# Optimization experiments

Measured on AMD Instinct MI355X. Metric: run time of the kernel, lower is better.

Reference implementation:

```python
import jax, jax.numpy as jnp
from jax import lax
import numpy as np

NSTEP, NGRID, MU = 365, 4000, 8
STAIND = NSTEP - 1          # time index providing static parameters
TDLST = [1, 2, 3, 4, 5]     # 1-based indices of dynamic parameters
HBV_LO = jnp.array([0.0, 1.0, 0.005, 0.005, 0.0, 0.0, 0.005, 0.005, 0.0, 0.0, 0.0], jnp.float32)
HBV_HI = jnp.array([1.0, 2000.0, 0.995, 0.995, 1.0, 7.0, 0.995, 0.995, 1.0, 1.0, 1.0], jnp.float32)
SMIN = 1e-4                 # clamp floor for states
CAPMIN = 0.005 / 4          # floor for derived capacities

# ---- MARRMoT-style flux helpers (all elementwise) ----

def split_1(p1, In):
    return p1 * In

def soilmoisture_1(S1, S1max, S2, S2max):
    mask = (S1 / S1max < S2 / S2max).astype(S1.dtype)
    return (S2 * S1max - S1 * S2max) / (S1max + S2max) * mask

def soilmoisture_2(S1, S1max, S2, S2max, S3, S3max):
    # water rebalance to equal relative storage (3 stores); flux drawn from S2
    mask = (S1 / S1max < (S2 + S3) / (S2max + S3max)).astype(S1.dtype)
    return (S2 * S1max - S1 * S2max) / (S1max + S2max + S3max) * mask

def evap_7(S, Smax, Ep, dt):
    return jnp.minimum(S / Smax * Ep, S / dt)

def evap_1(S, Ep, dt):
    return jnp.minimum(Ep, S / dt)

def saturation_1(In, S, Smax):
    return In * (S >= Smax).astype(In.dtype)

def interflow_5(p1, S):
    return p1 * S

def baseflow_1(p1, S):
    return p1 * S

def percolation_4(pbase, zperc, rexp, deficit, defmax, S, Smax, dt):
    pc = pbase * (1.0 + zperc * (deficit / defmax) ** (1.0 + rexp)) * S / Smax
    return jnp.maximum(0.0, jnp.minimum(pc, S / dt))

def deficit_dist(S1, S1max, S2, S2max):
    d1 = jnp.maximum(0.0, 1.0 - S1 / S1max)
    d2 = jnp.maximum(0.0, 1.0 - S2 / S2max)
    tot = d1 + d2
    return jnp.where(tot > 0, d1 / jnp.where(tot > 0, tot, 1.0), S1max / (S1max + S2max))


def _forward(x, parameters):
    Nstep, Ngrid = x.shape[0], x.shape[1]
    mu = parameters.shape[3]
    P_ = x[:, :, 0]   # [Nstep, Ngrid]
    Ep_ = x[:, :, 2]  # [Nstep, Ngrid]

    # scale raw [0,1] params to physical ranges
    parT = HBV_LO[None, None, :, None] + parameters * (HBV_HI - HBV_LO)[None, None, :, None]
    parsta = parT[STAIND]  # [Ngrid, 11, mu] static params
    dyn = np.zeros(11, dtype=bool)
    for ix in TDLST:
        dyn[ix - 1] = True
    dyn = jnp.asarray(dyn)
    # dydrop=0 -> dynamic params always used on tdlst slots, static elsewhere
    parhbv = jnp.where(dyn[None, None, :, None], parT, parsta[None])  # [Nstep,Ngrid,11,mu]

    S0 = jnp.full((Ngrid, mu), 0.001, x.dtype)

    def step(carry, inp):
        S1, S2, S3, S4, S5 = carry
        Pt, Ept, par = inp            # par: [Ngrid, 11, mu]
        P = Pt[:, None]               # [Ngrid, 1] broadcasts against [Ngrid, mu]
        Ep = Ept[:, None]
        pctim, smax, f1, f2, kuz, rexp, f3, f4, pfree, klzp, klzs = [par[:, i, :] for i in range(11)]

        uztwm = f1 * smax
        uzfwm = jnp.maximum(CAPMIN, f2 * (smax - uztwm))
        lztwm = jnp.maximum(CAPMIN, f3 * (smax - uztwm - uzfwm))
        lzfwpm = jnp.maximum(CAPMIN, f4 * (smax - uztwm - uzfwm - lztwm))
        lzfwsm = jnp.maximum(CAPMIN, (1.0 - f4) * (smax - uztwm - uzfwm - lztwm))
        pbase = lzfwpm * klzp + lzfwsm * klzs
        denom = lzfwsm * klzs + lzfwpm * klzp
        zperc = jnp.minimum(1e5, (lztwm + lzfwsm * (1.0 - klzs)) / denom + lzfwpm * (1.0 - klzp) / denom)
        dt = 1.0

        flux_qdir = split_1(pctim, P)
        flux_peff = split_1(1.0 - pctim, P)
        flux_ru = soilmoisture_1(S1, uztwm, S2, uzfwm)
        flux_euztw = evap_7(S1, uztwm, Ep, dt)
        flux_twexu = saturation_1(flux_peff, S1, uztwm)
        flux_qsur = saturation_1(flux_twexu, S2, uzfwm)
        flux_qint = interflow_5(kuz, S2)
        flux_euzfw = evap_1(S2, jnp.maximum(0.0, Ep - flux_euztw), dt)
        deficit = (jnp.maximum(1e-8, lztwm - S3) + jnp.maximum(1e-8, lzfwpm - S4)
                   + jnp.maximum(1e-8, lzfwsm - S5))
        defmax = jnp.maximum(1e-8, lztwm + lzfwpm + lzfwsm)
        flux_pc = percolation_4(pbase, zperc, rexp, deficit, defmax, S2, uzfwm, dt)
        flux_pctw = split_1(1.0 - pfree, flux_pc)
        flux_elztw = evap_7(S3, lztwm, jnp.maximum(0.0, Ep - flux_euztw - flux_euzfw), dt)
        flux_twexl = saturation_1(flux_pctw, S3, lztwm)
        fp = deficit_dist(S4, lzfwpm, S5, lzfwsm)
        fs = deficit_dist(S5, lzfwsm, S4, lzfwpm)
        flux_twexlp = split_1(fp, flux_twexl)
        flux_twexls = split_1(fs, flux_twexl)
        flux_pcfwp = split_1(pfree * fp, flux_pc)
        flux_pcfws = split_1(pfree * fs, flux_pc)
        flux_rlp = soilmoisture_2(S3, lztwm, S4, lzfwpm, S5, lzfwsm)
        flux_rls = soilmoisture_2(S3, lztwm, S5, lzfwsm, S4, lzfwpm)
        flux_qbfp = baseflow_1(klzp, S4)
        flux_qbfs = baseflow_1(klzs, S5)

        nS1 = jnp.maximum(S1 + flux_peff + flux_ru - flux_euztw - flux_twexu, SMIN)
        nS2 = jnp.maximum(S2 + flux_twexu - flux_euzfw - flux_qsur - flux_qint - flux_ru - flux_pc, SMIN)
        nS3 = jnp.maximum(S3 + flux_pctw + flux_rlp + flux_rls - flux_elztw - flux_twexl, SMIN)
        nS4 = jnp.maximum(S4 + flux_twexlp + flux_pcfwp - flux_rlp - flux_qbfp, SMIN)
        nS5 = jnp.maximum(S5 + flux_twexls + flux_pcfws - flux_rls - flux_qbfs, SMIN)

        qsim = flux_qdir + flux_qsur + flux_qint + flux_qbfp + flux_qbfs
        et = flux_euztw + flux_euzfw + flux_elztw
        return (nS1, nS2, nS3, nS4, nS5), (qsim, et)

    _, (Qsimmu, ETmu) = lax.scan(step, (S0, S0, S0, S0, S0), (P_, Ep_, parhbv))
    Qs = Qsimmu.mean(-1, keepdims=True)      # muwts=None -> mean over components
    ETave = ETmu.mean(-1, keepdims=True)
    return jnp.concatenate([Qs, ETave], axis=-1)  # [Nstep, Ngrid, 2]


def setup_inputs() -> dict:
    key = jax.random.key(0)
    k1, k2 = jax.random.split(key)
    x = jax.random.uniform(k1, (NSTEP, NGRID, 3), dtype=jnp.float32)
    parameters = jax.random.uniform(k2, (NSTEP, NGRID, 11, MU), dtype=jnp.float32)
    return {"x": x, "parameters": parameters}


def reference(x, parameters):
    return _forward(x, parameters)
```

## Files before the change

### kernel.cpp

```cpp
#include <hip/hip_runtime.h>
#include <stdint.h>

#define NSTEP 365
#define NGRID 4000
#define CAPMIN 0.00125f
#define SMINV 0.0001f
#define PSTR_DW (NGRID * 88)
#define XSTR_DW (NGRID * 3)

#define RAW_SLOT 384
#define RAW_REG  (5 * RAW_SLOT)
#define DER_BASE 7680
#define DER_SLOT 768
#define DER_REG  (5 * DER_SLOT)
#define SMQ_BASE 15360
#define SME_BASE 15680

typedef __attribute__((address_space(3))) uint32_t lds_u32_t;
typedef __attribute__((address_space(1))) uint32_t glb_u32_t;

__device__ __forceinline__ void dma4(const float* g, float* l) {
    __builtin_amdgcn_global_load_lds((const glb_u32_t*)(const void*)g,
                                     (lds_u32_t*)(void*)l, 4, 0, 0);
}

__device__ __forceinline__ float frcp(float x) { return __builtin_amdgcn_rcpf(x); }
__device__ __forceinline__ float fexp2(float x) { return __builtin_amdgcn_exp2f(x); }
__device__ __forceinline__ float flog2(float x) { return __builtin_amdgcn_logf(x); }

__device__ __forceinline__ void issue_slot(const float* pp, const float* px,
                                           int t, float* dst) {
    const float* pj = pp + (size_t)t * PSTR_DW;
    dma4(pj,      dst);
    dma4(pj + 8,  dst + 64);
    dma4(pj + 16, dst + 128);
    dma4(pj + 24, dst + 192);
    dma4(pj + 32, dst + 256);
    dma4(px + (size_t)t * XSTR_DW, dst + 320);
}

#define RDS(j)                                                               \
    const float  c0_##j = rreg[(j) * RAW_SLOT + lane];                       \
    const float  kz_##j = rreg[(j) * RAW_SLOT + 256 + lane];                 \
    const float  Pp_##j = rreg[(j) * RAW_SLOT + 320 + gl3];                  \
    const float  Ee_##j = rreg[(j) * RAW_SLOT + 322 + gl3];                  \
    const float2 dA_##j = dreg[(j) * 384 + lane];                            \
    const float2 dB_##j = dreg[(j) * 384 + 64 + lane];                       \
    const float2 dC_##j = dreg[(j) * 384 + 128 + lane];                      \
    const float2 dD_##j = dreg[(j) * 384 + 192 + lane];                      \
    const float2 dE_##j = dreg[(j) * 384 + 256 + lane];                      \
    const float2 dF_##j = dreg[(j) * 384 + 320 + lane];

#define STEP(j) do {                                                         \
    const float uztwm = dA_##j.x, uzfwm = dA_##j.y;                          \
    const float inv_uztwm = dB_##j.x, inv_uzfwm = dB_##j.y;                  \
    const float inv_uzsum = dC_##j.x, lztwm = dC_##j.y;                      \
    const float inv_lztwm = dD_##j.x, pbase = dD_##j.y;                      \
    const float lzfwpm = dE_##j.x, lzfwsm = dE_##j.y;                        \
    const float pz = dF_##j.x, inv_defmax = dF_##j.y;                        \
    const float Ep = Ee_##j, kuz = kz_##j;                                   \
    const float qdir = c0_##j * Pp_##j;                                      \
    const float peff = Pp_##j - qdir;                                        \
    const float rud  = S2 * uztwm - S1 * uzfwm;                              \
    const float ru   = (rud > 0.0f) ? rud * inv_uzsum : 0.0f;                \
    const float euztw = fminf(S1 * inv_uztwm * Ep, S1);                      \
    const float twexu = (S1 >= uztwm) ? peff : 0.0f;                         \
    const float qsur  = (S2 >= uzfwm) ? twexu : 0.0f;                        \
    const float qint  = kuz * S2;                                            \
    const float euzfw = fminf(fmaxf(0.0f, Ep - euztw), S2);                  \
    const float deficit = fmaxf(1e-8f, lztwm - S3)                           \
                        + fmaxf(1e-8f, lzfwpm - S4)                          \
                        + fmaxf(1e-8f, lzfwsm - S5);                         \
    const float powterm = fexp2(e1 * flog2(deficit * inv_defmax));           \
    float pc = (pbase + pz * powterm) * (S2 * inv_uzfwm);                    \
    pc = fmaxf(0.0f, fminf(pc, S2));                                         \
    const float pctw  = (1.0f - pfree) * pc;                                 \
    const float elztw = fminf(S3 * inv_lztwm                                 \
                              * fmaxf(0.0f, Ep - euztw - euzfw), S3);        \
    const float twexl = (S3 >= lztwm) ? pctw : 0.0f;                         \
    const float aa  = fmaxf(0.0f, lzfwpm - S4) * lzfwsm;                     \
    const float bb  = fmaxf(0.0f, lzfwsm - S5) * lzfwpm;                     \
    const float den = aa + bb;                                               \
    const float pm  = lzfwpm + lzfwsm;                                       \
    const float fp  = ((den > 0.0f) ? aa : lzfwpm)                           \
                    * frcp((den > 0.0f) ? den : pm);                         \
    const float fs  = 1.0f - fp;                                             \
    const float twexlp = fp * twexl;                                         \
    const float twexls = fs * twexl;                                         \
    const float pcfwp  = pfree * fp * pc;                                    \
    const float pcfws  = pfree * fs * pc;                                    \
    const bool rlm = S3 * pm < (S4 + S5) * lztwm;                            \
    const float rlp = rlm ? (S4 * lztwm - S3 * lzfwpm) * inv_defmax : 0.0f;  \
    const float rls = rlm ? (S5 * lztwm - S3 * lzfwsm) * inv_defmax : 0.0f;  \
    const float qbfp = klzp * S4;                                            \
    const float qbfs = klzs * S5;                                            \
    S1 = fmaxf(S1 + peff + ru - euztw - twexu, SMINV);                       \
    S2 = fmaxf(S2 + twexu - euzfw - qsur - qint - ru - pc, SMINV);           \
    S3 = fmaxf(S3 + pctw + rlp + rls - elztw - twexl, SMINV);                \
    S4 = fmaxf(S4 + twexlp + pcfwp - rlp - qbfp, SMINV);                     \
    S5 = fmaxf(S5 + twexls + pcfws - rls - qbfs, SMINV);                     \
    smq[(j) * 64 + lane] = qdir + qsur + qint + qbfp + qbfs;                 \
    sme[(j) * 64 + lane] = euztw + euzfw + elztw;                            \
} while (0)

__global__ __launch_bounds__(192, 1) void sacsma_kernel(
    const float* __restrict__ x,
    const float* __restrict__ par,
    float* __restrict__ out)
{
    __shared__ __align__(16) float lds[16000];

    const int wave = threadIdx.x >> 6;
    const int lane = threadIdx.x & 63;
    const int g0   = blockIdx.x * 8;
    const int gl   = lane >> 3;
    const int mu   = lane & 7;
    const int g    = g0 + gl;

    if (wave == 0) {
        const float* pp = par + (size_t)g * 88 + mu;
        int xl = lane; if (xl >= 24) xl -= 24; if (xl >= 24) xl -= 24;
        const int xq = xl / 3;
        const float* px = x + (g0 + xq) * 3 + (xl - xq * 3);

        #pragma unroll
        for (int j = 0; j < 5; ++j)
            issue_slot(pp, px, j, lds + j * RAW_SLOT);

        for (int i = 0; i < 75; ++i) {
            if (i <= 71) {
                const int b = i + 1;
                float* dst = lds + (b & 3) * RAW_REG;
                const int tb = 5 * b;
                #pragma unroll
                for (int j = 0; j < 5; ++j)
                    issue_slot(pp, px, tb + j, dst + j * RAW_SLOT);
                asm volatile("s_waitcnt vmcnt(30)" ::: "memory");
            } else {
                asm volatile("s_waitcnt vmcnt(0)" ::: "memory");
            }
            asm volatile("s_barrier" ::: "memory");
        }
    } else if (wave == 1) {
        const float* ps = par + ((size_t)(NSTEP - 1) * NGRID + g) * 88 + mu;
        const float f3   = 0.005f + ps[6 * 8] * 0.99f;
        const float f4   = 0.005f + ps[7 * 8] * 0.99f;
        const float klzp = ps[9 * 8];
        const float klzs = ps[10 * 8];

        for (int i = 0; i < 75; ++i) {
            if (i >= 1 && i <= 73) {
                const int b = i - 1;
                const float* rreg = lds + (b & 3) * RAW_REG;
                float* dregf = lds + DER_BASE + (b & 1) * DER_REG;
                #pragma unroll
                for (int j = 0; j < 5; ++j) {
                    const float* rb = rreg + j * RAW_SLOT;
                    float2* db = reinterpret_cast<float2*>(dregf + j * DER_SLOT);

                    const float c1 = rb[64 + lane];
                    const float c2 = rb[128 + lane];
                    const float c3 = rb[192 + lane];

                    const float smaxv = 1.0f + c1 * 1999.0f;
                    const float f1 = 0.005f + c2 * 0.99f;
                    const float f2 = 0.005f + c3 * 0.99f;
                    const float uztwm = f1 * smaxv;
                    float rem = smaxv - uztwm;
                    const float uzfwm = fmaxf(CAPMIN, f2 * rem);
                    rem -= uzfwm;
                    const float lztwm = fmaxf(CAPMIN, f3 * rem);
                    rem -= lztwm;
                    const float lzfwpm = fmaxf(CAPMIN, f4 * rem);
                    const float lzfwsm = fmaxf(CAPMIN, (1.0f - f4) * rem);
                    const float pbase = lzfwpm * klzp + lzfwsm * klzs;
                    const float pz = fminf(lztwm + lzfwsm * (1.0f - klzs)
                                           + lzfwpm * (1.0f - klzp),
                                           100000.0f * pbase);
                    const float inv_uztwm = frcp(uztwm);
                    const float inv_uzfwm = frcp(uzfwm);
                    const float inv_lztwm = frcp(lztwm);
                    const float inv_uzsum = frcp(uztwm + uzfwm);
                    const float inv_defmax = frcp(lztwm + lzfwpm + lzfwsm);

                    db[0 * 64 + lane] = make_float2(uztwm, uzfwm);
                    db[1 * 64 + lane] = make_float2(inv_uztwm, inv_uzfwm);
                    db[2 * 64 + lane] = make_float2(inv_uzsum, lztwm);
                    db[3 * 64 + lane] = make_float2(inv_lztwm, pbase);
                    db[4 * 64 + lane] = make_float2(lzfwpm, lzfwsm);
                    db[5 * 64 + lane] = make_float2(pz, inv_defmax);
                }
                asm volatile("s_waitcnt lgkmcnt(0)" ::: "memory");
            }
            asm volatile("s_barrier" ::: "memory");
        }
    } else {
        const float* ps = par + ((size_t)(NSTEP - 1) * NGRID + g) * 88 + mu;
        const float e1    = 1.0f + ps[5 * 8] * 7.0f;
        const float pfree = ps[8 * 8];
        const float klzp  = ps[9 * 8];
        const float klzs  = ps[10 * 8];

        float S1 = 0.001f, S2 = 0.001f, S3 = 0.001f, S4 = 0.001f, S5 = 0.001f;
        float* smq = lds + SMQ_BASE;
        float* sme = lds + SME_BASE;
        const int gl3 = gl * 3;

        for (int i = 0; i < 75; ++i) {
            if (i >= 2) {
                const int b = i - 2;
                const float* rreg = lds + (b & 3) * RAW_REG;
                const float2* dreg = reinterpret_cast<const float2*>(
                    lds + DER_BASE + (b & 1) * DER_REG);

                RDS(0) RDS(1) RDS(2) RDS(3) RDS(4)
                STEP(0); STEP(1); STEP(2); STEP(3); STEP(4);

                if (lane < 40) {
                    const int s  = lane >> 3;
                    const int gg = lane & 7;
                    const float4* q4 = reinterpret_cast<const float4*>(&smq[s * 64 + gg * 8]);
                    const float4* e4 = reinterpret_cast<const float4*>(&sme[s * 64 + gg * 8]);
                    const float4 qa = q4[0], qb = q4[1];
                    const float4 ea = e4[0], eb = e4[1];
                    const float qsum = ((qa.x + qa.y) + (qa.z + qa.w))
                                     + ((qb.x + qb.y) + (qb.z + qb.w));
                    const float esum = ((ea.x + ea.y) + (ea.z + ea.w))
                                     + ((eb.x + eb.y) + (eb.z + eb.w));
                    float2 o = make_float2(qsum * 0.125f, esum * 0.125f);
                    *reinterpret_cast<float2*>(
                        out + ((size_t)(5 * b + s) * NGRID + g0 + gg) * 2) = o;
                }
            }
            asm volatile("s_barrier" ::: "memory");
        }
    }
}

extern "C" void kernel_launch(void* const* d_in, const int* in_sizes, int n_in,
                              void* d_out, int out_size, void* d_ws, size_t ws_size,
                              hipStream_t stream) {
    const float* x   = (const float*)d_in[0];
    const float* par = (const float*)d_in[1];
    float* out = (float*)d_out;

    sacsma_kernel<<<NGRID / 8, 192, 0, stream>>>(x, par, out);
}
```

Baseline: 106.5 us.

## Move output reduction to loader wave, compact x DMA, set wave priorities

The per-batch mean-over-mu reduction and global store move from the serial compute wave to the loader wave. They read a double-buffered LDS staging area three iterations later. The x forcing loads are packed into two DMA instructions per batch instead of five, with a tighter LDS layout, and wave priorities are set so the compute wave gets issue preference. A redundant fmax(0) clamp on percolation is dropped. This shortens the critical recurrence path, at the cost of more complex LDS buffer lifetimes and a final drain store.

New measurement: 128.2 us (median of 2 runs). 20.4% more time.

```diff
diff --git a/kernel.cpp b/kernel.cpp
--- a/kernel.cpp
+++ b/kernel.cpp
@@ -8,13 +8,13 @@
 #define PSTR_DW (NGRID * 88)
 #define XSTR_DW (NGRID * 3)
 
-#define RAW_SLOT 384
-#define RAW_REG  (5 * RAW_SLOT)
-#define DER_BASE 7680
+#define RAW_REG  1728
+#define X_OFF    1600
+#define DER_BASE 6912
 #define DER_SLOT 768
-#define DER_REG  (5 * DER_SLOT)
-#define SMQ_BASE 15360
-#define SME_BASE 15680
+#define DER_REG  3840
+#define STG_BASE 14592
+#define STG_REG  640
 
 typedef __attribute__((address_space(3))) uint32_t lds_u32_t;
 typedef __attribute__((address_space(1))) uint32_t glb_u32_t;
@@ -28,22 +28,11 @@
 __device__ __forceinline__ float fexp2(float x) { return __builtin_amdgcn_exp2f(x); }
 __device__ __forceinline__ float flog2(float x) { return __builtin_amdgcn_logf(x); }
 
-__device__ __forceinline__ void issue_slot(const float* pp, const float* px,
-                                           int t, float* dst) {
-    const float* pj = pp + (size_t)t * PSTR_DW;
-    dma4(pj,      dst);
-    dma4(pj + 8,  dst + 64);
-    dma4(pj + 16, dst + 128);
-    dma4(pj + 24, dst + 192);
-    dma4(pj + 32, dst + 256);
-    dma4(px + (size_t)t * XSTR_DW, dst + 320);
-}
-
 #define RDS(j)                                                               \
-    const float  c0_##j = rreg[(j) * RAW_SLOT + lane];                       \
-    const float  kz_##j = rreg[(j) * RAW_SLOT + 256 + lane];                 \
-    const float  Pp_##j = rreg[(j) * RAW_SLOT + 320 + gl3];                  \
-    const float  Ee_##j = rreg[(j) * RAW_SLOT + 322 + gl3];                  \
+    const float  c0_##j = rreg[(j) * 320 + lane];                            \
+    const float  kz_##j = rreg[(j) * 320 + 256 + lane];                      \
+    const float  Pp_##j = xreg[(j) * 24 + gl3];                              \
+    const float  Ee_##j = xreg[(j) * 24 + gl3 + 2];                          \
     const float2 dA_##j = dreg[(j) * 384 + lane];                            \
     const float2 dB_##j = dreg[(j) * 384 + 64 + lane];                       \
     const float2 dC_##j = dreg[(j) * 384 + 128 + lane];                      \
@@ -72,8 +61,7 @@
                         + fmaxf(1e-8f, lzfwpm - S4)                          \
                         + fmaxf(1e-8f, lzfwsm - S5);                         \
     const float powterm = fexp2(e1 * flog2(deficit * inv_defmax));           \
-    float pc = (pbase + pz * powterm) * (S2 * inv_uzfwm);                    \
-    pc = fmaxf(0.0f, fminf(pc, S2));                                         \
+    const float pc = fminf((pbase + pz * powterm) * (S2 * inv_uzfwm), S2);   \
     const float pctw  = (1.0f - pfree) * pc;                                 \
     const float elztw = fminf(S3 * inv_lztwm                                 \
                               * fmaxf(0.0f, Ep - euztw - euzfw), S3);        \
@@ -99,8 +87,8 @@
     S3 = fmaxf(S3 + pctw + rlp + rls - elztw - twexl, SMINV);                \
     S4 = fmaxf(S4 + twexlp + pcfwp - rlp - qbfp, SMINV);                     \
     S5 = fmaxf(S5 + twexls + pcfws - rls - qbfs, SMINV);                     \
-    smq[(j) * 64 + lane] = qdir + qsur + qint + qbfp + qbfs;                 \
-    sme[(j) * 64 + lane] = euztw + euzfw + elztw;                            \
+    stq[(j) * 64 + lane] = qdir + qsur + qint + qbfp + qbfs;                 \
+    stq[320 + (j) * 64 + lane] = euztw + euzfw + elztw;                      \
 } while (0)
 
 __global__ __launch_bounds__(192, 1) void sacsma_kernel(
@@ -108,7 +96,7 @@
     const float* __restrict__ par,
     float* __restrict__ out)
 {
-    __shared__ __align__(16) float lds[16000];
+    __shared__ __align__(16) float lds[15872];
 
     const int wave = threadIdx.x >> 6;
     const int lane = threadIdx.x & 63;
@@ -118,30 +106,69 @@
     const int g    = g0 + gl;
 
     if (wave == 0) {
+        __builtin_amdgcn_s_setprio(0);
         const float* pp = par + (size_t)g * 88 + mu;
-        int xl = lane; if (xl >= 24) xl -= 24; if (xl >= 24) xl -= 24;
-        const int xq = xl / 3;
-        const float* px = x + (g0 + xq) * 3 + (xl - xq * 3);
-
-        #pragma unroll
-        for (int j = 0; j < 5; ++j)
-            issue_slot(pp, px, j, lds + j * RAW_SLOT);
-
-        for (int i = 0; i < 75; ++i) {
-            if (i <= 71) {
-                const int b = i + 1;
-                float* dst = lds + (b & 3) * RAW_REG;
-                const int tb = 5 * b;
-                #pragma unroll
-                for (int j = 0; j < 5; ++j)
-                    issue_slot(pp, px, tb + j, dst + j * RAW_SLOT);
-                asm volatile("s_waitcnt vmcnt(30)" ::: "memory");
+        const int tA = lane / 24;
+        const int rA = lane - 24 * tA;
+        int idxB = lane + 64;
+        int tB = idxB / 24;
+        int rB = idxB - 24 * tB;
+        if (tB > 4) { tB = 4; rB = idxB - 120; }
+        const float* pxA = x + (size_t)tA * XSTR_DW + g0 * 3 + rA;
+        const float* pxB = x + (size_t)tB * XSTR_DW + g0 * 3 + rB;
+
+        #define ISSUE_BATCH(b) do {                                          \
+            float* reg_ = lds + ((b) & 3) * RAW_REG;                         \
+            const int tb_ = 5 * (b);                                         \
+            _Pragma("unroll")                                                \
+            for (int j = 0; j < 5; ++j) {                                    \
+                const float* pj_ = pp + (size_t)(tb_ + j) * PSTR_DW;         \
+                float* dst_ = reg_ + j * 320;                                \
+                dma4(pj_,      dst_);                                        \
+                dma4(pj_ + 8,  dst_ + 64);                                   \
+                dma4(pj_ + 16, dst_ + 128);                                  \
+                dma4(pj_ + 24, dst_ + 192);                                  \
+                dma4(pj_ + 32, dst_ + 256);                                  \
+            }                                                                \
+            dma4(pxA + (size_t)tb_ * XSTR_DW, reg_ + X_OFF);                 \
+            dma4(pxB + (size_t)tb_ * XSTR_DW, reg_ + X_OFF + 64);            \
+        } while (0)
+
+        #define REDUCE_STORE(b) do {                                         \
+            if (lane < 40) {                                                 \
+                const float* stg_ = lds + STG_BASE + ((b) & 1) * STG_REG;    \
+                const int s_  = lane >> 3;                                   \
+                const int gg_ = lane & 7;                                    \
+                const float4 qa = *(const float4*)&stg_[s_ * 64 + gg_ * 8];  \
+                const float4 qb = *(const float4*)&stg_[s_ * 64 + gg_ * 8 + 4];\
+                const float4 ea = *(const float4*)&stg_[320 + s_ * 64 + gg_ * 8];\
+                const float4 eb = *(const float4*)&stg_[320 + s_ * 64 + gg_ * 8 + 4];\
+                const float qsum = ((qa.x + qa.y) + (qa.z + qa.w))           \
+                                 + ((qb.x + qb.y) + (qb.z + qb.w));          \
+                const float esum = ((ea.x + ea.y) + (ea.z + ea.w))           \
+                                 + ((eb.x + eb.y) + (eb.z + eb.w));          \
+                float2 o = make_float2(qsum * 0.125f, esum * 0.125f);        \
+                *reinterpret_cast<float2*>(                                   \
+                    out + ((size_t)(5 * (b) + s_) * NGRID + g0 + gg_) * 2) = o;\
+            }                                                                \
+        } while (0)
+
+        ISSUE_BATCH(0);
+
+        for (int ip = 0; ip < 75; ++ip) {
+            if (ip >= 3)
+                REDUCE_STORE(ip - 3);
+            if (ip <= 71) {
+                ISSUE_BATCH(ip + 1);
+                asm volatile("s_waitcnt vmcnt(27)" ::: "memory");
             } else {
                 asm volatile("s_waitcnt vmcnt(0)" ::: "memory");
             }
             asm volatile("s_barrier" ::: "memory");
         }
+        REDUCE_STORE(72);
     } else if (wave == 1) {
+        __builtin_amdgcn_s_setprio(1);
         const float* ps = par + ((size_t)(NSTEP - 1) * NGRID + g) * 88 + mu;
         const float f3   = 0.005f + ps[6 * 8] * 0.99f;
         const float f4   = 0.005f + ps[7 * 8] * 0.99f;
@@ -155,7 +182,7 @@
                 float* dregf = lds + DER_BASE + (b & 1) * DER_REG;
                 #pragma unroll
                 for (int j = 0; j < 5; ++j) {
-                    const float* rb = rreg + j * RAW_SLOT;
+                    const float* rb = rreg + j * 320;
                     float2* db = reinterpret_cast<float2*>(dregf + j * DER_SLOT);
 
                     const float c1 = rb[64 + lane];
@@ -195,6 +222,7 @@
             asm volatile("s_barrier" ::: "memory");
         }
     } else {
+        __builtin_amdgcn_s_setprio(2);
         const float* ps = par + ((size_t)(NSTEP - 1) * NGRID + g) * 88 + mu;
         const float e1    = 1.0f + ps[5 * 8] * 7.0f;
         const float pfree = ps[8 * 8];
@@ -202,35 +230,21 @@
         const float klzs  = ps[10 * 8];
 
         float S1 = 0.001f, S2 = 0.001f, S3 = 0.001f, S4 = 0.001f, S5 = 0.001f;
-        float* smq = lds + SMQ_BASE;
-        float* sme = lds + SME_BASE;
         const int gl3 = gl * 3;
 
         for (int i = 0; i < 75; ++i) {
             if (i >= 2) {
                 const int b = i - 2;
                 const float* rreg = lds + (b & 3) * RAW_REG;
+                const float* xreg = rreg + X_OFF;
                 const float2* dreg = reinterpret_cast<const float2*>(
                     lds + DER_BASE + (b & 1) * DER_REG);
+                float* stq = lds + STG_BASE + (b & 1) * STG_REG;
 
                 RDS(0) RDS(1) RDS(2) RDS(3) RDS(4)
                 STEP(0); STEP(1); STEP(2); STEP(3); STEP(4);
 
-                if (lane < 40) {
-                    const int s  = lane >> 3;
-                    const int gg = lane & 7;
-                    const float4* q4 = reinterpret_cast<const float4*>(&smq[s * 64 + gg * 8]);
-                    const float4* e4 = reinterpret_cast<const float4*>(&sme[s * 64 + gg * 8]);
-                    const float4 qa = q4[0], qb = q4[1];
-                    const float4 ea = e4[0], eb = e4[1];
-                    const float qsum = ((qa.x + qa.y) + (qa.z + qa.w))
-                                     + ((qb.x + qb.y) + (qb.z + qb.w));
-                    const float esum = ((ea.x + ea.y) + (ea.z + ea.w))
-                                     + ((eb.x + eb.y) + (eb.z + eb.w));
-                    float2 o = make_float2(qsum * 0.125f, esum * 0.125f);
-                    *reinterpret_cast<float2*>(
-                        out + ((size_t)(5 * b + s) * NGRID + g0 + gg) * 2) = o;
-                }
+                asm volatile("s_waitcnt lgkmcnt(0)" ::: "memory");
             }
             asm volatile("s_barrier" ::: "memory");
         }
```
